# Kernel tuning notes

Hardware: AMD Instinct MI355X
Metric: run time of the kernel (lower is better)

The kernel has to match this reference:

```python
import jax, jax.numpy as jnp
import numpy as np

S = 2048      # sequence length (prefill, start_idx=0)
D = 4096      # model dim
H = 32        # query heads
KVH = 8       # kv heads (GQA)
HD = D // H   # head dim = 128
ROPE_BASE = 500000.0  # llama3 rope theta
NEG = -1e9    # additive causal mask value (finite stand-in for -inf)


def setup_inputs() -> dict:
    key = jax.random.key(0)
    ks = jax.random.split(key, 5)
    scale = 1.0 / np.sqrt(D)
    x = jax.random.normal(ks[0], (S, D), jnp.float32)
    wq = jax.random.normal(ks[1], (D, D), jnp.float32) * scale
    wk = jax.random.normal(ks[2], (KVH * HD, D), jnp.float32) * scale
    wv = jax.random.normal(ks[3], (KVH * HD, D), jnp.float32) * scale
    wo = jax.random.normal(ks[4], (D, D), jnp.float32) * scale
    # RoPE tables, [S, HD//2]
    pos = jnp.arange(S, dtype=jnp.float32)
    inv_freq = 1.0 / (ROPE_BASE ** (jnp.arange(0, HD, 2, dtype=jnp.float32) / HD))
    ang = pos[:, None] * inv_freq[None, :]
    freqs_cos = jnp.cos(ang)
    freqs_sin = jnp.sin(ang)
    # additive causal mask [S, S]
    mask = jnp.where(jnp.tril(jnp.ones((S, S), bool)), 0.0, NEG).astype(jnp.float32)
    return dict(x=x, wq=wq, wk=wk, wv=wv, wo=wo, mask=mask,
                freqs_cos=freqs_cos, freqs_sin=freqs_sin)


def _rope(t, cos, sin):
    # t: [S, nh, hd]; cos/sin: [S, hd//2] -> interleaved even/odd rotation
    even = t[:, :, 0::2]
    odd = t[:, :, 1::2]
    c = cos[:, None, :]
    s = sin[:, None, :]
    re = even * c - odd * s
    im = even * s + odd * c
    return jnp.stack([re, im], axis=-1).reshape(t.shape)


def reference(x, wq, wk, wv, wo, mask, freqs_cos, freqs_sin):
    s, d = x.shape
    q = (x @ wq.T).reshape(s, H, HD)
    k = (x @ wk.T).reshape(s, KVH, HD)
    v = (x @ wv.T).reshape(s, KVH, HD)
    q = _rope(q, freqs_cos, freqs_sin)
    k = _rope(k, freqs_cos, freqs_sin)
    # KV-cache append at start_idx=0 then read back == identity (prefill)
    # GQA: repeat_interleave kv heads to match query heads
    k = jnp.repeat(k, H // KVH, axis=1)  # [s, H, HD]
    v = jnp.repeat(v, H // KVH, axis=1)
    logits = jnp.einsum('qhd,khd->hqk', q, k) * (1.0 / np.sqrt(HD)) + mask[None]
    p = jax.nn.softmax(logits, axis=-1)
    o = jnp.einsum('hqk,khd->qhd', p, v).reshape(s, d)
    return o @ wo.T
```

## Files before the change

### kernel.cpp

```cpp
#include <hip/hip_runtime.h>
#include <hip/hip_bf16.h>
#include <stdint.h>

#define S2   2048
#define DD   4096
#define NH   32
#define NKVH 8
#define HD2  128
#define QKVW 6144

typedef __bf16 bf16x8 __attribute__((ext_vector_type(8)));
typedef float  f32x4  __attribute__((ext_vector_type(4)));
typedef unsigned short u16x8 __attribute__((ext_vector_type(8)));
typedef unsigned short u16x4 __attribute__((ext_vector_type(4)));

__device__ __forceinline__ unsigned short f2b(float f) {
    unsigned int u = __builtin_bit_cast(unsigned int, f);
    unsigned int r = (u + 0x7FFFu + ((u >> 16) & 1u)) >> 16;
    return (unsigned short)r;
}
__device__ __forceinline__ float b2f(unsigned short h) {
    unsigned int u = ((unsigned int)h) << 16;
    return __builtin_bit_cast(float, u);
}
__device__ __forceinline__ unsigned cvt_pk_bf16(float a, float b) {
    unsigned r;
    asm("v_cvt_pk_bf16_f32 %0, %1, %2" : "=v"(r) : "v"(a), "v"(b));
    return r;
}

__device__ __forceinline__ void gload_lds16(const void* g, void* lds) {
    __builtin_amdgcn_global_load_lds(
        (const __attribute__((address_space(1))) void*)(uintptr_t)g,
        (__attribute__((address_space(3))) void*)(uint32_t)(uintptr_t)lds,
        16, 0, 0);
}

#define BAR() do { asm volatile("" ::: "memory"); \
                   __builtin_amdgcn_s_barrier();  \
                   asm volatile("" ::: "memory"); } while (0)
#define WAITV(n) asm volatile("s_waitcnt vmcnt(" #n ")" ::: "memory")

template<int N> __device__ __forceinline__ void waitv() {
    if      constexpr (N == 0)  WAITV(0);
    else if constexpr (N == 2)  WAITV(2);
    else if constexpr (N == 4)  WAITV(4);
    else if constexpr (N == 6)  WAITV(6);
    else if constexpr (N == 8)  WAITV(8);
    else if constexpr (N == 10) WAITV(10);
    else if constexpr (N == 12) WAITV(12);
}

__global__ void cvt_all(const float* __restrict__ x,  const float* __restrict__ wq,
                        const float* __restrict__ wk, const float* __restrict__ wv,
                        const float* __restrict__ wo, unsigned short* __restrict__ dst) {
    const long long NG = 12LL * 1024 * 1024;
    const long long stride = (long long)gridDim.x * blockDim.x;
    for (long long g = (long long)blockIdx.x * blockDim.x + threadIdx.x; g < NG; g += stride) {
        const float* src; long long off;
        if      (g < 2LL*1024*1024) { src = x;  off = g; }
        else if (g < 6LL*1024*1024) { src = wq; off = g - 2LL*1024*1024; }
        else if (g < 7LL*1024*1024) { src = wk; off = g - 6LL*1024*1024; }
        else if (g < 8LL*1024*1024) { src = wv; off = g - 7LL*1024*1024; }
        else                        { src = wo; off = g - 8LL*1024*1024; }
        f32x4 v = *reinterpret_cast<const f32x4*>(src + off * 4);
        u16x4 o;
        o[0] = f2b(v[0]); o[1] = f2b(v[1]); o[2] = f2b(v[2]); o[3] = f2b(v[3]);
        *reinterpret_cast<u16x4*>(dst + g * 4) = o;
    }
}

template<int BN, int NW, typename CT>
__global__ __launch_bounds__(NW * 64) void gemm256(
    const unsigned short* __restrict__ A,
    const unsigned short* __restrict__ B0,
    const unsigned short* __restrict__ B1,
    const unsigned short* __restrict__ B2,
    int nb0, int nb01,
    CT* __restrict__ C, int ldc)
{
    constexpr int K = 4096, BK = 64, NT = K / BK;
    constexpr int NWC = NW / 2;
    constexpr int LA = 16 / NW;
    constexpr int LB = 2;
    __shared__ unsigned short As[2][256 * 64];
    __shared__ unsigned short Bs[2][BN * 64];

    const int bm = blockIdx.y, bn = blockIdx.x;
    const int tid = threadIdx.x;
    const int w = tid >> 6, lane = tid & 63;
    const int wr = w / NWC, wc = w % NWC;
    const int r16 = lane & 15, g4 = lane >> 4;

    const int bn0 = bn * BN;
    const unsigned short* Bp;
    if      (bn0 < nb0)  Bp = B0 + (size_t)bn0 * K;
    else if (bn0 < nb01) Bp = B1 + (size_t)(bn0 - nb0) * K;
    else                 Bp = B2 + (size_t)(bn0 - nb01) * K;
    const unsigned short* Ap = A + (size_t)bm * 256 * K;

    const int lrow = lane >> 3;
    const int lchk = lane & 7;

    f32x4 acc[8][4] = {};
    bf16x8 af[4][2], b0[2][2], b1[2][2];

    auto stageA = [&](int buf, int tt, int half) {
        #pragma unroll
        for (int i = 0; i < LA; ++i) {
            const int s  = i * NW + w;
            const int rb = ((s & 7) * 8) + ((s >> 3) * 128) + half * 64;
            const int row = rb + lrow;
            gload_lds16(Ap + (size_t)row * K + tt * BK + ((lchk ^ (row & 7)) * 8),
                        &As[buf][rb * 64]);
        }
    };
    auto stageB = [&](int buf, int tt, int half) {
        #pragma unroll
        for (int i = 0; i < 2; ++i) {
            const int s  = i * NW + w;
            const int rb = ((s & 3) * 8) + ((s >> 2) * 64) + half * 32;
            const int row = rb + lrow;
            gload_lds16(Bp + (size_t)row * K + tt * BK + ((lchk ^ (row & 7)) * 8),
                        &Bs[buf][rb * 64]);
        }
    };
    auto readA = [&](int buf, int mh) {
        #pragma unroll
        for (int m = 0; m < 4; ++m)
            #pragma unroll
            for (int kk = 0; kk < 2; ++kk) {
                const int row = wr * 128 + mh * 64 + m * 16 + r16;
                af[m][kk] = *reinterpret_cast<const bf16x8*>(
                    &As[buf][row * 64 + (((kk * 4 + g4) ^ (row & 7)) * 8)]);
            }
    };
    auto readB = [&](int buf, int nh, bf16x8 (&br)[2][2]) {
        #pragma unroll
        for (int n = 0; n < 2; ++n)
            #pragma unroll
            for (int kk = 0; kk < 2; ++kk) {
                const int row = wc * 64 + nh * 32 + n * 16 + r16;
                br[n][kk] = *reinterpret_cast<const bf16x8*>(
                    &Bs[buf][row * 64 + (((kk * 4 + g4) ^ (row & 7)) * 8)]);
            }
    };
    auto mma = [&](bf16x8 (&br)[2][2], int mh, int nh) {
        __builtin_amdgcn_s_setprio(1);
        #pragma unroll
        for (int m = 0; m < 4; ++m)
            #pragma unroll
            for (int n = 0; n < 2; ++n)
                #pragma unroll
                for (int kk = 0; kk < 2; ++kk)
                    acc[mh * 4 + m][nh * 2 + n] = __builtin_amdgcn_mfma_f32_16x16x32_bf16(
                        af[m][kk], br[n][kk], acc[mh * 4 + m][nh * 2 + n], 0, 0, 0);
        __builtin_amdgcn_s_setprio(0);
    };

    stageA(0, 0, 0); stageB(0, 0, 0); stageB(0, 0, 1); stageA(0, 0, 1);
    waitv<LA + LB>();
    BAR();

    for (int t = 0; t < NT - 1; ++t) {
        const int buf = t & 1;
        readA(buf, 0); readB(buf, 0, b0);
        stageA(buf ^ 1, t + 1, 0); stageB(buf ^ 1, t + 1, 0);
        BAR();
        mma(b0, 0, 0);
        waitv<2 * LA + LB>();
        BAR();
        readB(buf, 1, b1);
        stageB(buf ^ 1, t + 1, 1);
        BAR();
        mma(b1, 0, 1);
        waitv<LA + 2 * LB>();
        BAR();
        readA(buf, 1);
        stageA(buf ^ 1, t + 1, 1);
        BAR();
        mma(b1, 1, 1);
        BAR();
        mma(b0, 1, 0);
        waitv<LA + LB>();
        BAR();
    }
    {
        const int buf = (NT - 1) & 1;
        readA(buf, 0); readB(buf, 0, b0);
        BAR();
        mma(b0, 0, 0);
        waitv<LA>();
        BAR();
        readB(buf, 1, b1);
        mma(b1, 0, 1);
        waitv<0>();
        readA(buf, 1);
        mma(b1, 1, 1);
        mma(b0, 1, 0);
    }

    const size_t crow0 = (size_t)bm * 256 + wr * 128;
    const size_t ccol0 = (size_t)bn * BN + wc * 64;
    #pragma unroll
    for (int m = 0; m < 8; ++m)
        #pragma unroll
        for (int n = 0; n < 4; ++n)
            #pragma unroll
            for (int r = 0; r < 4; ++r) {
                const size_t row = crow0 + m * 16 + g4 * 4 + r;
                const size_t col = ccol0 + n * 16 + r16;
                if constexpr (sizeof(CT) == 2) C[row * ldc + col] = (CT)f2b(acc[m][n][r]);
                else                           C[row * ldc + col] = (CT)acc[m][n][r];
            }
}

__global__ __launch_bounds__(512) void gemm_wo(
    const unsigned short* __restrict__ A,
    const unsigned short* __restrict__ B,
    float* __restrict__ C, int ldc)
{
    constexpr int K = 4096, BK = 64, NT = K / BK;
    __shared__ unsigned short As[3][256 * BK];
    __shared__ unsigned short Bs[3][128 * BK];

    const int bm = blockIdx.y, bn = blockIdx.x;
    const int tid = threadIdx.x;
    const int w = tid >> 6, lane = tid & 63;
    const int wr = w >> 1, wc = w & 1;
    const int r16 = lane & 15, g4 = lane >> 4;

    const unsigned short* Ap = A + (size_t)bm * 256 * K;
    const unsigned short* Bp = B + (size_t)bn * 128 * K;

    const int lrow = lane >> 3;
    const int lchk = lane & 7;

    f32x4 acc[4][4] = {};

    auto stage = [&](int slot, int tt) {
        #pragma unroll
        for (int i = 0; i < 4; ++i) {
            const int u = i * 8 + w;
            const int row = u * 8 + lrow;
            gload_lds16(Ap + (size_t)row * K + tt * BK + ((lchk ^ (row & 7)) * 8),
                        &As[slot][u * 512]);
        }
        #pragma unroll
        for (int i = 0; i < 2; ++i) {
            const int u = i * 8 + w;
            const int row = u * 8 + lrow;
            gload_lds16(Bp + (size_t)row * K + tt * BK + ((lchk ^ (row & 7)) * 8),
                        &Bs[slot][u * 512]);
        }
    };

    stage(0, 0);
    stage(1, 1);
    waitv<6>();
    BAR();

    int rs_ = 0, ws_ = 2;
    for (int t = 0; t < NT; ++t) {
        bf16x8 af[4][2], bfr[4][2];
        #pragma unroll
        for (int m = 0; m < 4; ++m)
            #pragma unroll
            for (int kk = 0; kk < 2; ++kk) {
                const int row = wr * 64 + m * 16 + r16;
                af[m][kk] = *reinterpret_cast<const bf16x8*>(
                    &As[rs_][row * BK + (((kk * 4 + g4) ^ (row & 7)) * 8)]);
            }
        #pragma unroll
        for (int n = 0; n < 4; ++n)
            #pragma unroll
            for (int kk = 0; kk < 2; ++kk) {
                const int row = wc * 64 + n * 16 + r16;
                bfr[n][kk] = *reinterpret_cast<const bf16x8*>(
                    &Bs[rs_][row * BK + (((kk * 4 + g4) ^ (row & 7)) * 8)]);
            }
        if (t + 2 < NT) stage(ws_, t + 2);
        __builtin_amdgcn_s_setprio(1);
        #pragma unroll
        for (int m = 0; m < 4; ++m)
            #pragma unroll
            for (int n = 0; n < 4; ++n)
                #pragma unroll
                for (int kk = 0; kk < 2; ++kk)
                    acc[m][n] = __builtin_amdgcn_mfma_f32_16x16x32_bf16(
                        af[m][kk], bfr[n][kk], acc[m][n], 0, 0, 0);
        __builtin_amdgcn_s_setprio(0);
        if (t + 2 < NT) waitv<6>(); else waitv<0>();
        BAR();
        rs_ = (rs_ == 2) ? 0 : rs_ + 1;
        ws_ = (ws_ == 2) ? 0 : ws_ + 1;
    }

    const size_t crow0 = (size_t)bm * 256 + wr * 64;
    const size_t ccol0 = (size_t)bn * 128 + wc * 64;
    #pragma unroll
    for (int m = 0; m < 4; ++m)
        #pragma unroll
        for (int n = 0; n < 4; ++n)
            #pragma unroll
            for (int r = 0; r < 4; ++r)
                C[(crow0 + m * 16 + g4 * 4 + r) * ldc + ccol0 + n * 16 + r16] = acc[m][n][r];
}

__global__ __launch_bounds__(256) void rope_kernel(unsigned short* __restrict__ qkv,
                                                   const float* __restrict__ fc,
                                                   const float* __restrict__ fs) {
    constexpr float QSCALE = 0.08838834764831845f * 1.4426950408889634f;
    const int g = blockIdx.x * 256 + threadIdx.x;
    if (g >= 640) return;
    const int s = blockIdx.y;
    const int col = g * 8;
    unsigned short* p = qkv + (size_t)s * QKVW + col;
    u16x8 v = *reinterpret_cast<const u16x8*>(p);
    const int i0 = (col & 127) >> 1;
    f32x4 c  = *reinterpret_cast<const f32x4*>(fc + s * 64 + i0);
    f32x4 sn = *reinterpret_cast<const f32x4*>(fs + s * 64 + i0);
    const float post = (col < DD) ? QSCALE : 1.0f;
    u16x8 o;
    #pragma unroll
    for (int j = 0; j < 4; ++j) {
        float e  = b2f(v[2*j]);
        float od = b2f(v[2*j+1]);
        o[2*j]   = f2b((e * c[j] - od * sn[j]) * post);
        o[2*j+1] = f2b((e * sn[j] + od * c[j]) * post);
    }
    *reinterpret_cast<u16x8*>(p) = o;
}

__global__ __launch_bounds__(256) void transpose_v(const unsigned short* __restrict__ qkv,
                                                   unsigned short* __restrict__ Vt) {
    __shared__ unsigned short tile[64][72];
    const int d0g = blockIdx.x * 64;
    const int s0  = blockIdx.y * 64;
    const int kvh = d0g >> 7, dl0 = d0g & 127;
    const int tid = threadIdx.x;
    #pragma unroll
    for (int p = 0; p < 2; ++p) {
        const int sgi = p * 256 + tid;
        const int srow = sgi >> 3, dseg = sgi & 7;
        u16x8 v = *reinterpret_cast<const u16x8*>(
            qkv + (size_t)(s0 + srow) * QKVW + 5120 + d0g + dseg * 8);
        #pragma unroll
        for (int j = 0; j < 8; ++j) tile[srow][dseg * 8 + j] = v[j];
    }
    __syncthreads();
    #pragma unroll
    for (int p = 0; p < 2; ++p) {
        const int sgi = p * 256 + tid;
        const int drow = sgi >> 3, sseg = sgi & 7;
        u16x8 v;
        #pragma unroll
        for (int j = 0; j < 8; ++j) v[j] = tile[sseg * 8 + j][drow];
        *reinterpret_cast<u16x8*>(
            Vt + (size_t)kvh * HD2 * S2 + (size_t)(dl0 + drow) * S2 + s0 + sseg * 8) = v;
    }
}

__global__ __launch_bounds__(256) void attn_kernel(const unsigned short* __restrict__ Qkv,
                                                   const unsigned short* __restrict__ Vt,
                                                   unsigned short* __restrict__ O) {
    __shared__ unsigned short Klds[2][64 * 128];
    __shared__ unsigned short Vlds[2][128 * 64];
    __shared__ unsigned short Plds[4][2048];

    const int kvh = blockIdx.x;
    const int h   = kvh * 4 + (blockIdx.y & 3);
    const int c   = 15 - (blockIdx.y >> 2);
    const int w = threadIdx.x >> 6, lane = threadIdx.x & 63;
    const int r16 = lane & 15, g4 = lane >> 4;

    const int qw  = c * 128 + w * 32;
    const int ntB = 2 * c + 2;

    const unsigned short* Kbase = Qkv + DD + kvh * HD2;
    const unsigned short* Vtb   = Vt + (size_t)kvh * HD2 * S2;
    char* pw = (char*)(&Plds[w][0]);

    const int krow_l = lane >> 4;
    const int kchunk = lane & 15;
    const int vd_l   = lane >> 3;
    const int vchunk = lane & 7;

    bf16x8 qf[2][4];
    #pragma unroll
    for (int m = 0; m < 2; ++m)
        #pragma unroll
        for (int f = 0; f < 4; ++f)
            qf[m][f] = *reinterpret_cast<const bf16x8*>(
                Qkv + (size_t)(qw + m * 16 + r16) * QKVW + h * HD2 + f * 32 + g4 * 8);

    f32x4 o[2][8] = {};
    float mr[2] = {-3e38f, -3e38f};
    float lr[2] = {0.f, 0.f};

    auto stage = [&](int buf, int kv0) {
        #pragma unroll
        for (int i = 0; i < 4; ++i) {
            const int seg = i * 4 + w;
            const int row = seg * 4 + krow_l;
            gload_lds16(Kbase + (size_t)(kv0 + row) * QKVW + ((kchunk ^ (row & 7)) * 8),
                        &Klds[buf][seg * 512]);
        }
        #pragma unroll
        for (int i = 0; i < 4; ++i) {
            const int seg = i * 4 + w;
            const int d = seg * 8 + vd_l;
            gload_lds16(Vtb + (size_t)d * S2 + kv0 + ((vchunk ^ (d & 7)) * 8),
                        &Vlds[buf][seg * 512]);
        }
    };

    stage(0, 0);
    WAITV(0);
    __syncthreads();

    for (int t = 0; t < ntB; ++t) {
        const int buf = t & 1;
        const int kv0 = t * 64;
        if (t + 1 < ntB) stage(buf ^ 1, (t + 1) * 64);

        if (kv0 <= qw + 31) {
            f32x4 sa[2][4] = {};
            #pragma unroll
            for (int kb = 0; kb < 4; ++kb) {
                bf16x8 kf[4];
                #pragma unroll
                for (int f = 0; f < 4; ++f)
                    kf[f] = *reinterpret_cast<const bf16x8*>(
                        &Klds[buf][(kb * 16 + r16) * 128 + (((f * 4 + g4) ^ (r16 & 7)) * 8)]);
                __builtin_amdgcn_s_setprio(1);
                #pragma unroll
                for (int m = 0; m < 2; ++m)
                    #pragma unroll
                    for (int f = 0; f < 4; ++f)
                        sa[m][kb] = __builtin_amdgcn_mfma_f32_16x16x32_bf16(
                            kf[f], qf[m][f], sa[m][kb], 0, 0, 0);
                __builtin_amdgcn_s_setprio(0);
            }
            const bool needmask = (kv0 + 63 > qw);
            float sv[2][4][4];
            #pragma unroll
            for (int m = 0; m < 2; ++m)
                #pragma unroll
                for (int kb = 0; kb < 4; ++kb)
                    #pragma unroll
                    for (int r = 0; r < 4; ++r) {
                        float xx = sa[m][kb][r];
                        if (needmask) {
                            const int kvg = kv0 + kb * 16 + g4 * 4 + r;
                            const int qg  = qw + m * 16 + r16;
                            xx = (kvg > qg) ? -3e38f : xx;
                        }
                        sv[m][kb][r] = xx;
                    }
            float rowm[2];
            #pragma unroll
            for (int m = 0; m < 2; ++m) {
                float a0 = fmaxf(fmaxf(sv[m][0][0], sv[m][0][1]), fmaxf(sv[m][0][2], sv[m][0][3]));
                float a1 = fmaxf(fmaxf(sv[m][1][0], sv[m][1][1]), fmaxf(sv[m][1][2], sv[m][1][3]));
                float a2 = fmaxf(fmaxf(sv[m][2][0], sv[m][2][1]), fmaxf(sv[m][2][2], sv[m][2][3]));
                float a3 = fmaxf(fmaxf(sv[m][3][0], sv[m][3][1]), fmaxf(sv[m][3][2], sv[m][3][3]));
                rowm[m] = fmaxf(fmaxf(a0, a1), fmaxf(a2, a3));
            }
            #pragma unroll
            for (int m = 0; m < 2; ++m) {
                rowm[m] = fmaxf(rowm[m], __shfl_xor(rowm[m], 16));
                rowm[m] = fmaxf(rowm[m], __shfl_xor(rowm[m], 32));
            }
            const float gmax = fmaxf(rowm[0] - mr[0], rowm[1] - mr[1]);
            if (!__all(gmax <= 11.5f)) {
                float corr[2];
                #pragma unroll
                for (int m = 0; m < 2; ++m) {
                    const float mn = fmaxf(mr[m], rowm[m]);
                    corr[m] = exp2f(mr[m] - mn);
                    mr[m] = mn;
                    lr[m] *= corr[m];
                }
                #pragma unroll
                for (int m = 0; m < 2; ++m)
                    #pragma unroll
                    for (int r = 0; r < 4; ++r) {
                        const float co = __shfl(corr[m], (lane & 48) | (g4 * 4 + r));
                        #pragma unroll
                        for (int n = 0; n < 8; ++n) o[m][n][r] *= co;
                    }
            }
            float rs[2] = {0.f, 0.f};
            #pragma unroll
            for (int m = 0; m < 2; ++m)
                #pragma unroll
                for (int kb = 0; kb < 4; ++kb)
                    #pragma unroll
                    for (int r = 0; r < 4; ++r) {
                        const float pp = exp2f(sv[m][kb][r] - mr[m]);
                        sv[m][kb][r] = pp;
                        rs[m] += pp;
                    }
            #pragma unroll
            for (int m = 0; m < 2; ++m) {
                rs[m] += __shfl_xor(rs[m], 16);
                rs[m] += __shfl_xor(rs[m], 32);
                lr[m] += rs[m];
            }
            #pragma unroll
            for (int m = 0; m < 2; ++m)
                #pragma unroll
                for (int kb = 0; kb < 4; ++kb) {
                    const unsigned w0 = cvt_pk_bf16(sv[m][kb][0], sv[m][kb][1]);
                    const unsigned w1 = cvt_pk_bf16(sv[m][kb][2], sv[m][kb][3]);
                    int wa = m * 2048 + ((kb * 2) + (g4 >> 1)) * 256 + r16 * 16 + (g4 & 1) * 8;
                    wa ^= (r16 >> 3) << 4;
                    *reinterpret_cast<unsigned long long*>(pw + wa) =
                        (unsigned long long)w0 | ((unsigned long long)w1 << 32);
                }
            asm volatile("s_waitcnt lgkmcnt(0)" ::: "memory");
            bf16x8 pa[2][2];
            #pragma unroll
            for (int m = 0; m < 2; ++m)
                #pragma unroll
                for (int kvs = 0; kvs < 2; ++kvs) {
                    int ra = m * 2048 + kvs * 1024 + lane * 16;
                    ra ^= (r16 >> 3) << 4;
                    pa[m][kvs] = *reinterpret_cast<const bf16x8*>(pw + ra);
                }
            #pragma unroll
            for (int kvs = 0; kvs < 2; ++kvs)
                #pragma unroll
                for (int n = 0; n < 8; ++n) {
                    const bf16x8 vb = *reinterpret_cast<const bf16x8*>(
                        &Vlds[buf][(n * 16 + r16) * 64 + (((kvs * 4 + g4) ^ (r16 & 7)) * 8)]);
                    __builtin_amdgcn_s_setprio(1);
                    #pragma unroll
                    for (int m = 0; m < 2; ++m)
                        o[m][n] = __builtin_amdgcn_mfma_f32_16x16x32_bf16(
                            pa[m][kvs], vb, o[m][n], 0, 0, 0);
                    __builtin_amdgcn_s_setprio(0);
                }
        }

        WAITV(0);
        __syncthreads();
    }

    float inv[2];
    #pragma unroll
    for (int m = 0; m < 2; ++m) inv[m] = 1.0f / lr[m];
    #pragma unroll
    for (int m = 0; m < 2; ++m)
        #pragma unroll
        for (int r = 0; r < 4; ++r) {
            const float iv = __shfl(inv[m], (lane & 48) | (g4 * 4 + r));
            #pragma unroll
            for (int n = 0; n < 8; ++n)
                O[(size_t)(qw + m * 16 + g4 * 4 + r) * DD + h * HD2 + n * 16 + r16] =
                    f2b(o[m][n][r] * iv);
        }
}

extern "C" void kernel_launch(void* const* d_in, const int* in_sizes, int n_in,
                              void* d_out, int out_size, void* d_ws, size_t ws_size,
                              hipStream_t stream) {
    (void)in_sizes; (void)n_in; (void)out_size; (void)ws_size;
    const float* x  = (const float*)d_in[0];
    const float* wq = (const float*)d_in[1];
    const float* wk = (const float*)d_in[2];
    const float* wv = (const float*)d_in[3];
    const float* wo = (const float*)d_in[4];
    const float* fc = (const float*)d_in[6];
    const float* fs = (const float*)d_in[7];
    float* out = (float*)d_out;

    unsigned short* ws = (unsigned short*)d_ws;
    const size_t M1 = 1024 * 1024;
    unsigned short* xb  = ws;
    unsigned short* wqb = ws + 8  * M1;
    unsigned short* wkb = ws + 24 * M1;
    unsigned short* wvb = ws + 28 * M1;
    unsigned short* wob = ws + 32 * M1;
    unsigned short* qkv = ws + 48 * M1;
    unsigned short* vt  = ws + 60 * M1;
    unsigned short* ob  = ws + 62 * M1;

    cvt_all<<<2048, 256, 0, stream>>>(x, wq, wk, wv, wo, ws);
    gemm256<256, 8, unsigned short><<<dim3(24, 8), 512, 0, stream>>>(
        xb, wqb, wkb, wvb, 4096, 5120, qkv, QKVW);
    rope_kernel<<<dim3(3, 2048), 256, 0, stream>>>(qkv, fc, fs);
    transpose_v<<<dim3(16, 32), 256, 0, stream>>>(qkv, vt);
    attn_kernel<<<dim3(8, 64), 256, 0, stream>>>(qkv, vt, ob);
    gemm_wo<<<dim3(32, 8), 512, 0, stream>>>(ob, wob, out, DD);
}
```

Baseline: 319.6 us.

## Retile QKV and output GEMMs to fill all CUs with 256-block grids

The QKV projection GEMM switches from 256x256 tiles (192 blocks) to 256x192 tiles (256 blocks), with each B sub-tile able to straddle the wq/wk/wv boundaries via per-row base lookup. The output projection GEMM replaces its 256x128 triple-buffered loop with a 128x256 double-buffered, half-step pipelined schedule matching the QKV kernel. The aim is to fill the 256 CUs with one block each and balance the per-CU load, at the cost of smaller per-block reuse and a more intricate wait-count schedule.

```diff
diff --git a/kernel.cpp b/kernel.cpp
--- a/kernel.cpp
+++ b/kernel.cpp
@@ -43,12 +43,13 @@
 
 template<int N> __device__ __forceinline__ void waitv() {
     if      constexpr (N == 0)  WAITV(0);
+    else if constexpr (N == 1)  WAITV(1);
     else if constexpr (N == 2)  WAITV(2);
+    else if constexpr (N == 3)  WAITV(3);
     else if constexpr (N == 4)  WAITV(4);
+    else if constexpr (N == 5)  WAITV(5);
     else if constexpr (N == 6)  WAITV(6);
     else if constexpr (N == 8)  WAITV(8);
-    else if constexpr (N == 10) WAITV(10);
-    else if constexpr (N == 12) WAITV(12);
 }
 
 __global__ void cvt_all(const float* __restrict__ x,  const float* __restrict__ wq,
@@ -70,96 +71,95 @@
     }
 }
 
-template<int BN, int NW, typename CT>
-__global__ __launch_bounds__(NW * 64) void gemm256(
+__global__ __launch_bounds__(512) void gemm_qkv(
     const unsigned short* __restrict__ A,
     const unsigned short* __restrict__ B0,
     const unsigned short* __restrict__ B1,
     const unsigned short* __restrict__ B2,
-    int nb0, int nb01,
-    CT* __restrict__ C, int ldc)
+    unsigned short* __restrict__ C)
 {
     constexpr int K = 4096, BK = 64, NT = K / BK;
-    constexpr int NWC = NW / 2;
-    constexpr int LA = 16 / NW;
-    constexpr int LB = 2;
     __shared__ unsigned short As[2][256 * 64];
-    __shared__ unsigned short Bs[2][BN * 64];
+    __shared__ unsigned short Bs[2][192 * 64];
 
     const int bm = blockIdx.y, bn = blockIdx.x;
     const int tid = threadIdx.x;
     const int w = tid >> 6, lane = tid & 63;
-    const int wr = w / NWC, wc = w % NWC;
+    const int wr = w >> 1, wc = w & 1;
     const int r16 = lane & 15, g4 = lane >> 4;
 
-    const int bn0 = bn * BN;
-    const unsigned short* Bp;
-    if      (bn0 < nb0)  Bp = B0 + (size_t)bn0 * K;
-    else if (bn0 < nb01) Bp = B1 + (size_t)(bn0 - nb0) * K;
-    else                 Bp = B2 + (size_t)(bn0 - nb01) * K;
+    const int bn0 = bn * 192;
     const unsigned short* Ap = A + (size_t)bm * 256 * K;
 
     const int lrow = lane >> 3;
     const int lchk = lane & 7;
 
-    f32x4 acc[8][4] = {};
-    bf16x8 af[4][2], b0[2][2], b1[2][2];
+    f32x4 acc[4][6] = {};
+    bf16x8 af[2][2], b0[3][2], b1[3][2];
+
+    auto browbase = [&](int rowg) -> const unsigned short* {
+        if (rowg < 4096) return B0 + (size_t)rowg * K;
+        if (rowg < 5120) return B1 + (size_t)(rowg - 4096) * K;
+        return B2 + (size_t)(rowg - 5120) * K;
+    };
 
     auto stageA = [&](int buf, int tt, int half) {
         #pragma unroll
-        for (int i = 0; i < LA; ++i) {
-            const int s  = i * NW + w;
-            const int rb = ((s & 7) * 8) + ((s >> 3) * 128) + half * 64;
-            const int row = rb + lrow;
+        for (int i = 0; i < 2; ++i) {
+            const int j = i * 8 + w;
+            const int row0 = (j >> 2) * 64 + half * 32 + (j & 3) * 8;
+            const int row = row0 + lrow;
             gload_lds16(Ap + (size_t)row * K + tt * BK + ((lchk ^ (row & 7)) * 8),
-                        &As[buf][rb * 64]);
+                        &As[buf][row0 * 64]);
         }
     };
     auto stageB = [&](int buf, int tt, int half) {
         #pragma unroll
         for (int i = 0; i < 2; ++i) {
-            const int s  = i * NW + w;
-            const int rb = ((s & 3) * 8) + ((s >> 2) * 64) + half * 32;
-            const int row = rb + lrow;
-            gload_lds16(Bp + (size_t)row * K + tt * BK + ((lchk ^ (row & 7)) * 8),
-                        &Bs[buf][rb * 64]);
+            const int j = (i == 0) ? w : (8 + (w & 3));
+            const int row0 = (j < 6) ? (half * 48 + j * 8)
+                                     : (96 + half * 48 + (j - 6) * 8);
+            const int row = row0 + lrow;
+            const unsigned short* src = browbase(bn0 + row0) + (size_t)lrow * K;
+            gload_lds16(src + tt * BK + ((lchk ^ (row & 7)) * 8),
+                        &Bs[buf][row0 * 64]);
         }
     };
     auto readA = [&](int buf, int mh) {
         #pragma unroll
-        for (int m = 0; m < 4; ++m)
+        for (int m = 0; m < 2; ++m)
             #pragma unroll
             for (int kk = 0; kk < 2; ++kk) {
-                const int row = wr * 128 + mh * 64 + m * 16 + r16;
+                const int row = wr * 64 + mh * 32 + m * 16 + r16;
                 af[m][kk] = *reinterpret_cast<const bf16x8*>(
                     &As[buf][row * 64 + (((kk * 4 + g4) ^ (row & 7)) * 8)]);
             }
     };
-    auto readB = [&](int buf, int nh, bf16x8 (&br)[2][2]) {
-        #pragma unroll
-        for (int n = 0; n < 2; ++n)
+    auto readB = [&](int buf, int nh, bf16x8 (&br)[3][2]) {
+        #pragma unroll
+        for (int n = 0; n < 3; ++n)
             #pragma unroll
             for (int kk = 0; kk < 2; ++kk) {
-                const int row = wc * 64 + nh * 32 + n * 16 + r16;
+                const int row = wc * 96 + nh * 48 + n * 16 + r16;
                 br[n][kk] = *reinterpret_cast<const bf16x8*>(
                     &Bs[buf][row * 64 + (((kk * 4 + g4) ^ (row & 7)) * 8)]);
             }
     };
-    auto mma = [&](bf16x8 (&br)[2][2], int mh, int nh) {
+    auto mma = [&](bf16x8 (&br)[3][2], int mh, int nh) {
         __builtin_amdgcn_s_setprio(1);
         #pragma unroll
-        for (int m = 0; m < 4; ++m)
-            #pragma unroll
-            for (int n = 0; n < 2; ++n)
+        for (int m = 0; m < 2; ++m)
+            #pragma unroll
+            for (int n = 0; n < 3; ++n)
                 #pragma unroll
                 for (int kk = 0; kk < 2; ++kk)
-                    acc[mh * 4 + m][nh * 2 + n] = __builtin_amdgcn_mfma_f32_16x16x32_bf16(
-                        af[m][kk], br[n][kk], acc[mh * 4 + m][nh * 2 + n], 0, 0, 0);
+                    acc[mh * 2 + m][nh * 3 + n] = __builtin_amdgcn_mfma_f32_16x16x32_bf16(
+                        af[m][kk], br[n][kk], acc[mh * 2 + m][nh * 3 + n], 0, 0, 0);
         __builtin_amdgcn_s_setprio(0);
     };
 
     stageA(0, 0, 0); stageB(0, 0, 0); stageB(0, 0, 1); stageA(0, 0, 1);
-    waitv<LA + LB>();
+    waitv<4>();
     BAR();
 
     for (int t = 0; t < NT - 1; ++t) {
@@ -168,13 +168,13 @@
         stageA(buf ^ 1, t + 1, 0); stageB(buf ^ 1, t + 1, 0);
         BAR();
         mma(b0, 0, 0);
-        waitv<2 * LA + LB>();
+        waitv<6>();
         BAR();
         readB(buf, 1, b1);
         stageB(buf ^ 1, t + 1, 1);
         BAR();
         mma(b1, 0, 1);
-        waitv<LA + 2 * LB>();
+        waitv<6>();
         BAR();
         readA(buf, 1);
         stageA(buf ^ 1, t + 1, 1);
@@ -182,7 +182,7 @@
         mma(b1, 1, 1);
         BAR();
         mma(b0, 1, 0);
-        waitv<LA + LB>();
+        waitv<4>();
         BAR();
     }
     {
@@ -190,7 +190,7 @@
         readA(buf, 0); readB(buf, 0, b0);
         BAR();
         mma(b0, 0, 0);
-        waitv<LA>();
+        waitv<2>();
         BAR();
         readB(buf, 1, b1);
         mma(b1, 0, 1);
@@ -200,111 +200,143 @@
         mma(b0, 1, 0);
     }
 
-    const size_t crow0 = (size_t)bm * 256 + wr * 128;
-    const size_t ccol0 = (size_t)bn * BN + wc * 64;
-    #pragma unroll
-    for (int m = 0; m < 8; ++m)
-        #pragma unroll
-        for (int n = 0; n < 4; ++n)
-            #pragma unroll
-            for (int r = 0; r < 4; ++r) {
-                const size_t row = crow0 + m * 16 + g4 * 4 + r;
-                const size_t col = ccol0 + n * 16 + r16;
-                if constexpr (sizeof(CT) == 2) C[row * ldc + col] = (CT)f2b(acc[m][n][r]);
-                else                           C[row * ldc + col] = (CT)acc[m][n][r];
-            }
-}
-
-__global__ __launch_bounds__(512) void gemm_wo(
+    const size_t crow0 = (size_t)bm * 256 + wr * 64;
+    const size_t ccol0 = (size_t)bn0 + wc * 96;
+    #pragma unroll
+    for (int m = 0; m < 4; ++m)
+        #pragma unroll
+        for (int n = 0; n < 6; ++n)
+            #pragma unroll
+            for (int r = 0; r < 4; ++r)
+                C[(crow0 + m * 16 + g4 * 4 + r) * QKVW + ccol0 + n * 16 + r16] =
+                    f2b(acc[m][n][r]);
+}
+
+__global__ __launch_bounds__(512) void gemm_out(
     const unsigned short* __restrict__ A,
     const unsigned short* __restrict__ B,
-    float* __restrict__ C, int ldc)
+    float* __restrict__ C)
 {
     constexpr int K = 4096, BK = 64, NT = K / BK;
-    __shared__ unsigned short As[3][256 * BK];
-    __shared__ unsigned short Bs[3][128 * BK];
+    __shared__ unsigned short As[2][128 * 64];
+    __shared__ unsigned short Bs[2][256 * 64];
 
     const int bm = blockIdx.y, bn = blockIdx.x;
     const int tid = threadIdx.x;
     const int w = tid >> 6, lane = tid & 63;
-    const int wr = w >> 1, wc = w & 1;
+    const int wr = w >> 2, wc = w & 3;
     const int r16 = lane & 15, g4 = lane >> 4;
 
-    const unsigned short* Ap = A + (size_t)bm * 256 * K;
-    const unsigned short* Bp = B + (size_t)bn * 128 * K;
+    const unsigned short* Ap = A + (size_t)bm * 128 * K;
+    const unsigned short* Bp = B + (size_t)bn * 256 * K;
 
     const int lrow = lane >> 3;
     const int lchk = lane & 7;
 
     f32x4 acc[4][4] = {};
-
-    auto stage = [&](int slot, int tt) {
-        #pragma unroll
-        for (int i = 0; i < 4; ++i) {
-            const int u = i * 8 + w;
-            const int row = u * 8 + lrow;
-            gload_lds16(Ap + (size_t)row * K + tt * BK + ((lchk ^ (row & 7)) * 8),
-                        &As[slot][u * 512]);
+    bf16x8 af[2][2], b0[2][2], b1[2][2];
+
+    auto stageA = [&](int buf, int tt, int half) {
+        const int j = w;
+        const int row0 = (j >> 2) * 64 + half * 32 + (j & 3) * 8;
+        const int row = row0 + lrow;
+        gload_lds16(Ap + (size_t)row * K + tt * BK + ((lchk ^ (row & 7)) * 8),
+                    &As[buf][row0 * 64]);
+    };
+    auto stageB = [&](int buf, int tt, int half) {
+        #pragma unroll
+        for (int i = 0; i < 2; ++i) {
+            const int j = i * 8 + w;
+            const int row0 = (j >> 2) * 64 + half * 32 + (j & 3) * 8;
+            const int row = row0 + lrow;
+            gload_lds16(Bp + (size_t)row * K + tt * BK + ((lchk ^ (row & 7)) * 8),
+                        &Bs[buf][row0 * 64]);
         }
-        #pragma unroll
-        for (int i = 0; i < 2; ++i) {
-            const int u = i * 8 + w;
-            const int row = u * 8 + lrow;
-            gload_lds16(Bp + (size_t)row * K + tt * BK + ((lchk ^ (row & 7)) * 8),
-                        &Bs[slot][u * 512]);
-        }
-    };
-
-    stage(0, 0);
-    stage(1, 1);
-    waitv<6>();
+    };
+    auto readA = [&](int buf, int mh) {
+        #pragma unroll
+        for (int m = 0; m < 2; ++m)
+            #pragma unroll
+            for (int kk = 0; kk < 2; ++kk) {
+                const int row = wr * 64 + mh * 32 + m * 16 + r16;
+                af[m][kk] = *reinterpret_cast<const bf16x8*>(
+                    &As[buf][row * 64 + (((kk * 4 + g4) ^ (row & 7)) * 8)]);
+            }
+    };
+    auto readB = [&](int buf, int nh, bf16x8 (&br)[2][2]) {
+        #pragma unroll
+        for (int n = 0; n < 2; ++n)
+            #pragma unroll
+            for (int kk = 0; kk < 2; ++kk) {
+                const int row = wc * 64 + nh * 32 + n * 16 + r16;
+                br[n][kk] = *reinterpret_cast<const bf16x8*>(
+                    &Bs[buf][row * 64 + (((kk * 4 + g4) ^ (row & 7)) * 8)]);
+            }
+    };
+    auto mma = [&](bf16x8 (&br)[2][2], int mh, int nh) {
+        __builtin_amdgcn_s_setprio(1);
+        #pragma unroll
+        for (int m = 0; m < 2; ++m)
+            #pragma unroll
+            for (int n = 0; n < 2; ++n)
+                #pragma unroll
+                for (int kk = 0; kk < 2; ++kk)
+                    acc[mh * 2 + m][nh * 2 + n] = __builtin_amdgcn_mfma_f32_16x16x32_bf16(
+                        af[m][kk], br[n][kk], acc[mh * 2 + m][nh * 2 + n], 0, 0, 0);
+        __builtin_amdgcn_s_setprio(0);
+    };
+
+    stageA(0, 0, 0); stageB(0, 0, 0); stageB(0, 0, 1); stageA(0, 0, 1);
+    waitv<3>();
     BAR();
 
-    int rs_ = 0, ws_ = 2;
-    for (int t = 0; t < NT; ++t) {
-        bf16x8 af[4][2], bfr[4][2];
-        #pragma unroll
-        for (int m = 0; m < 4; ++m)
-            #pragma unroll
-            for (int kk = 0; kk < 2; ++kk) {
-                const int row = wr * 64 + m * 16 + r16;
-                af[m][kk] = *reinterpret_cast<const bf16x8*>(
-                    &As[rs_][row * BK + (((kk * 4 + g4) ^ (row & 7)) * 8)]);
-            }
+    for (int t = 0; t < NT - 1; ++t) {
+        const int buf = t & 1;
+        readA(buf, 0); readB(buf, 0, b0);
+        stageA(buf ^ 1, t + 1, 0); stageB(buf ^ 1, t + 1, 0);
+        BAR();
+        mma(b0, 0, 0);
+        waitv<4>();
+        BAR();
+        readB(buf, 1, b1);
+        stageB(buf ^ 1, t + 1, 1);
+        BAR();
+        mma(b1, 0, 1);
+        waitv<5>();
+        BAR();
+        readA(buf, 1);
+        stageA(buf ^ 1, t + 1, 1);
+        BAR();
+        mma(b1, 1, 1);
+        BAR();
+        mma(b0, 1, 0);
+        waitv<3>();
+        BAR();
+    }
+    {
+        const int buf = (NT - 1) & 1;
+        readA(buf, 0); readB(buf, 0, b0);
+        BAR();
+        mma(b0, 0, 0);
+        waitv<1>();
+        BAR();
+        readB(buf, 1, b1);
+        mma(b1, 0, 1);
+        waitv<0>();
+        readA(buf, 1);
+        mma(b1, 1, 1);
+        mma(b0, 1, 0);
+    }
+
+    const size_t crow0 = (size_t)bm * 128 + wr * 64;
+    const size_t ccol0 = (size_t)bn * 256 + wc * 64;
+    #pragma unroll
+    for (int m = 0; m < 4; ++m)
         #pragma unroll
         for (int n = 0; n < 4; ++n)
             #pragma unroll
-            for (int kk = 0; kk < 2; ++kk) {
-                const int row = wc * 64 + n * 16 + r16;
-                bfr[n][kk] = *reinterpret_cast<const bf16x8*>(
-                    &Bs[rs_][row * BK + (((kk * 4 + g4) ^ (row & 7)) * 8)]);
-            }
-        if (t + 2 < NT) stage(ws_, t + 2);
-        __builtin_amdgcn_s_setprio(1);
-        #pragma unroll
-        for (int m = 0; m < 4; ++m)
-            #pragma unroll
-            for (int n = 0; n < 4; ++n)
-                #pragma unroll
-                for (int kk = 0; kk < 2; ++kk)
-                    acc[m][n] = __builtin_amdgcn_mfma_f32_16x16x32_bf16(
-                        af[m][kk], bfr[n][kk], acc[m][n], 0, 0, 0);
-        __builtin_amdgcn_s_setprio(0);
-        if (t + 2 < NT) waitv<6>(); else waitv<0>();
-        BAR();
-        rs_ = (rs_ == 2) ? 0 : rs_ + 1;
-        ws_ = (ws_ == 2) ? 0 : ws_ + 1;
-    }
-
-    const size_t crow0 = (size_t)bm * 256 + wr * 64;
-    const size_t ccol0 = (size_t)bn * 128 + wc * 64;
-    #pragma unroll
-    for (int m = 0; m < 4; ++m)
-        #pragma unroll
-        for (int n = 0; n < 4; ++n)
-            #pragma unroll
             for (int r = 0; r < 4; ++r)
-                C[(crow0 + m * 16 + g4 * 4 + r) * ldc + ccol0 + n * 16 + r16] = acc[m][n][r];
+                C[(crow0 + m * 16 + g4 * 4 + r) * DD + ccol0 + n * 16 + r16] = acc[m][n][r];
 }
 
 __global__ __launch_bounds__(256) void rope_kernel(unsigned short* __restrict__ qkv,
@@ -588,10 +620,9 @@
     unsigned short* ob  = ws + 62 * M1;
 
     cvt_all<<<2048, 256, 0, stream>>>(x, wq, wk, wv, wo, ws);
-    gemm256<256, 8, unsigned short><<<dim3(24, 8), 512, 0, stream>>>(
-        xb, wqb, wkb, wvb, 4096, 5120, qkv, QKVW);
+    gemm_qkv<<<dim3(32, 8), 512, 0, stream>>>(xb, wqb, wkb, wvb, qkv);
     rope_kernel<<<dim3(3, 2048), 256, 0, stream>>>(qkv, fc, fs);
     transpose_v<<<dim3(16, 32), 256, 0, stream>>>(qkv, vt);
     attn_kernel<<<dim3(8, 64), 256, 0, stream>>>(qkv, vt, ob);
-    gemm_wo<<<dim3(32, 8), 512, 0, stream>>>(ob, wob, out, DD);
-}
+    gemm_out<<<dim3(16, 16), 512, 0, stream>>>(ob, wob, out);
+}
```

Result: faster. 312.9 us (-2.1%).
